# Kernel optimization log

Hardware: AMD Instinct MI355X
Metric: run time of the kernel (lower is better)

The kernel has to match this reference:

```python
import jax, jax.numpy as jnp
from jax import lax
import numpy as np
import math

EMBED_DIM = 1024
NUM_HEADS = 16
REDUCTION = 2


def setup_inputs() -> dict:
    key = jax.random.key(0)
    ks = jax.random.split(key, 11)
    B, N, C = 2, 4096, EMBED_DIM
    s = 1.0 / math.sqrt(C)
    return {
        "x": jax.random.normal(ks[0], (B, N, C), jnp.float32),
        "q_w": jax.random.normal(ks[1], (C, C), jnp.float32) * s,
        "q_b": jax.random.normal(ks[2], (C,), jnp.float32) * s,
        "k_w": jax.random.normal(ks[3], (C, C), jnp.float32) * s,
        "k_b": jax.random.normal(ks[4], (C,), jnp.float32) * s,
        "v_w": jax.random.normal(ks[5], (C, C), jnp.float32) * s,
        "v_b": jax.random.normal(ks[6], (C,), jnp.float32) * s,
        "conv_w": jax.random.normal(ks[7], (C, 1, 3), jnp.float32) * 0.5,
        "conv_b": jax.random.normal(ks[8], (C,), jnp.float32) * 0.1,
        "out_w": jax.random.normal(ks[9], (C, C), jnp.float32) * s,
        "out_b": jax.random.normal(ks[10], (C,), jnp.float32) * s,
    }


def reference(x, q_w, q_b, k_w, k_b, v_w, v_b, conv_w, conv_b, out_w, out_b):
    B, N, C = x.shape
    H = NUM_HEADS
    D = C // H
    scale = 1.0 / math.sqrt(D)

    q = x @ q_w.T + q_b  # [B,N,C]

    # depthwise conv1d KV downsample: kernel=3, stride=REDUCTION, pad=1, groups=C
    xd = jnp.transpose(x, (0, 2, 1))  # [B,C,N]
    xd = lax.conv_general_dilated(
        xd, conv_w, window_strides=(REDUCTION,), padding=[(1, 1)],
        feature_group_count=C, dimension_numbers=("NCH", "OIH", "NCH"))
    xd = xd + conv_b[None, :, None]
    xd = jnp.transpose(xd, (0, 2, 1))  # [B,Nk,C]

    k = xd @ k_w.T + k_b
    v = xd @ v_w.T + v_b

    Nk = k.shape[1]
    q = q.reshape(B, N, H, D).transpose(0, 2, 1, 3)   # [B,H,N,D]
    k = k.reshape(B, Nk, H, D).transpose(0, 2, 1, 3)  # [B,H,Nk,D]
    v = v.reshape(B, Nk, H, D).transpose(0, 2, 1, 3)

    att = jnp.einsum("bhnd,bhmd->bhnm", q, k) * scale  # [B,H,N,Nk]
    att = jax.nn.softmax(att, axis=-1)
    out = jnp.einsum("bhnm,bhmd->bhnd", att, v)        # [B,H,N,D]
    out = out.transpose(0, 2, 1, 3).reshape(B, N, C)
    return out @ out_w.T + out_b
```

## Files before the change

### kernel.cpp

```cpp
#include <hip/hip_runtime.h>
#include <stdint.h>
#include <stddef.h>


using bf16x8 = __attribute__((ext_vector_type(8))) short;
using f32x4  = __attribute__((ext_vector_type(4))) float;
using f32x16 = __attribute__((ext_vector_type(16))) float;
using u16x4  = __attribute__((ext_vector_type(4))) unsigned short;
using u32x4  = __attribute__((ext_vector_type(4))) uint32_t;

#if defined(__has_builtin)
#if __has_builtin(__builtin_amdgcn_exp2f)
#define FAST_EXP2(x) __builtin_amdgcn_exp2f(x)
#endif
#endif
#ifndef FAST_EXP2
extern "C" __device__ float __ocml_native_exp2_f32(float);
#define FAST_EXP2(x) __ocml_native_exp2_f32(x)
#endif

__device__ __forceinline__ unsigned short f2bf(float f) {
  union { float f; uint32_t u; } v; v.f = f;
  uint32_t r = v.u + 0x7fffu + ((v.u >> 16) & 1u);
  return (unsigned short)(r >> 16);
}

__device__ __forceinline__ uint32_t cvt_pk_bf16(float lo, float hi) {
  uint32_t r;
  asm("v_cvt_pk_bf16_f32 %0, %1, %2" : "=v"(r) : "v"(lo), "v"(hi));
  return r;
}

__device__ __forceinline__ void plane32_swap(uint32_t& a, uint32_t& b) {
  asm("v_permlane32_swap_b32 %0, %1" : "+v"(a), "+v"(b));
}

__global__ __launch_bounds__(256)
void cast_bf16_kernel(const float* __restrict__ in, unsigned short* __restrict__ out, int n) {
  int i = (blockIdx.x * 256 + threadIdx.x) * 8;
  if (i >= n) return;
  float4 a = *(const float4*)(in + i);
  float4 b = *(const float4*)(in + i + 4);
  u16x4 r0 = {f2bf(a.x), f2bf(a.y), f2bf(a.z), f2bf(a.w)};
  u16x4 r1 = {f2bf(b.x), f2bf(b.y), f2bf(b.z), f2bf(b.w)};
  *(u16x4*)(out + i) = r0;
  *(u16x4*)(out + i + 4) = r1;
}

struct WPtrs { const float* p0; const float* p1; const float* p2; const float* p3; };
__global__ __launch_bounds__(256)
void cast4_bf16_kernel(WPtrs in, unsigned short* __restrict__ out) {
  int which = blockIdx.x >> 9;
  int i = ((blockIdx.x & 511) * 256 + threadIdx.x) * 8;
  const float* src = (which == 0) ? in.p0 : (which == 1) ? in.p1
                   : (which == 2) ? in.p2 : in.p3;
  unsigned short* dst = out + (size_t)which * 1048576;
  float4 a = *(const float4*)(src + i);
  float4 b = *(const float4*)(src + i + 4);
  u16x4 r0 = {f2bf(a.x), f2bf(a.y), f2bf(a.z), f2bf(a.w)};
  u16x4 r1 = {f2bf(b.x), f2bf(b.y), f2bf(b.z), f2bf(b.w)};
  *(u16x4*)(dst + i) = r0;
  *(u16x4*)(dst + i + 4) = r1;
}

__global__ __launch_bounds__(256)
void conv_ds_kernel(const float* __restrict__ x, const float* __restrict__ cw,
                    const float* __restrict__ cb, unsigned short* __restrict__ xd) {
  int row = blockIdx.x;
  int b = row >> 11, m = row & 2047;
  int c = threadIdx.x * 4;
  const float* xb = x + (size_t)b * 4096 * 1024;
  int n0 = 2 * m - 1;
  float4 x0 = {0.f, 0.f, 0.f, 0.f};
  if (n0 >= 0) x0 = *(const float4*)(xb + (size_t)n0 * 1024 + c);
  float4 x1 = *(const float4*)(xb + (size_t)(2 * m) * 1024 + c);
  float4 x2 = *(const float4*)(xb + (size_t)(2 * m + 1) * 1024 + c);
  float4 w0 = *(const float4*)(cw + c * 3);
  float4 w1 = *(const float4*)(cw + c * 3 + 4);
  float4 w2 = *(const float4*)(cw + c * 3 + 8);
  float4 bb = *(const float4*)(cb + c);
  float r0 = x0.x * w0.x + x1.x * w0.y + x2.x * w0.z + bb.x;
  float r1 = x0.y * w0.w + x1.y * w1.x + x2.y * w1.y + bb.y;
  float r2 = x0.z * w1.z + x1.z * w1.w + x2.z * w2.x + bb.z;
  float r3 = x0.w * w2.y + x1.w * w2.z + x2.w * w2.w + bb.w;
  u16x4 r = {f2bf(r0), f2bf(r1), f2bf(r2), f2bf(r3)};
  *(u16x4*)(xd + (size_t)row * 1024 + c) = r;
}

template<int OUT_MODE>
__global__ __launch_bounds__(256)
void gemm_bt(const unsigned short* __restrict__ A, const unsigned short* __restrict__ W,
             const float* __restrict__ bias, const float* __restrict__ bias2,
             void* __restrict__ out, void* __restrict__ out2,
             int M, int N, int K) {
  __shared__ unsigned short As[128 * 32];
  __shared__ unsigned short Bs[128 * 32];
  const int tid = threadIdx.x;
  const int w = tid >> 6, lane = tid & 63;
  const int nbn = N >> 7;
  const int bm = blockIdx.x / nbn, bn = blockIdx.x % nbn;
  const int wr = w >> 1, wc = w & 1;
  const int l15 = lane & 15, l4 = lane >> 4;

  f32x4 acc[4][4];
#pragma unroll
  for (int m = 0; m < 4; ++m)
#pragma unroll
    for (int n = 0; n < 4; ++n) acc[m][n] = (f32x4)0.0f;

  const int arow = bm * 128 + w * 16 + (lane >> 2);
  const int brow = bn * 128 + w * 16 + (lane >> 2);
  const int kcol = (lane & 3) * 8;

  for (int kt = 0; kt < K; kt += 32) {
#pragma unroll
    for (int p = 0; p < 2; ++p) {
      __builtin_amdgcn_global_load_lds(
          (const __attribute__((address_space(1))) void*)(A + (size_t)(arow + p * 64) * K + kt + kcol),
          (__attribute__((address_space(3))) void*)(As + p * 2048 + w * 512), 16, 0, 0);
      __builtin_amdgcn_global_load_lds(
          (const __attribute__((address_space(1))) void*)(W + (size_t)(brow + p * 64) * K + kt + kcol),
          (__attribute__((address_space(3))) void*)(Bs + p * 2048 + w * 512), 16, 0, 0);
    }
    __syncthreads();
    bf16x8 af[4], bf[4];
#pragma unroll
    for (int m = 0; m < 4; ++m) af[m] = *(const bf16x8*)(As + (wr * 64 + m * 16 + l15) * 32 + l4 * 8);
#pragma unroll
    for (int n = 0; n < 4; ++n) bf[n] = *(const bf16x8*)(Bs + (wc * 64 + n * 16 + l15) * 32 + l4 * 8);
#pragma unroll
    for (int m = 0; m < 4; ++m)
#pragma unroll
      for (int n = 0; n < 4; ++n)
        acc[m][n] = __builtin_amdgcn_mfma_f32_16x16x32_bf16(af[m], bf[n], acc[m][n], 0, 0, 0);
    __syncthreads();
  }

  const bool vregion = (OUT_MODE == 3) && (bn >= 8);
#pragma unroll
  for (int n = 0; n < 4; ++n) {
    int col = bn * 128 + wc * 64 + n * 16 + l15;
    float bv = vregion ? bias2[col - 1024] : bias[col];
#pragma unroll
    for (int m = 0; m < 4; ++m) {
      int row0 = bm * 128 + wr * 64 + m * 16 + l4 * 4;
      if (vregion) {
        int b = row0 >> 11, kv = row0 & 2047;
        u16x4 r = {f2bf(acc[m][n][0] + bv), f2bf(acc[m][n][1] + bv),
                   f2bf(acc[m][n][2] + bv), f2bf(acc[m][n][3] + bv)};
        *(u16x4*)((unsigned short*)out2 + ((size_t)(b * 1024 + (col - 1024))) * 2048 + kv) = r;
      } else if (OUT_MODE == 1 || OUT_MODE == 3) {
        const int ldn = (OUT_MODE == 3) ? 1024 : N;
#pragma unroll
        for (int i = 0; i < 4; ++i)
          ((unsigned short*)out)[(size_t)(row0 + i) * ldn + col] = f2bf(acc[m][n][i] + bv);
      } else {
#pragma unroll
        for (int i = 0; i < 4; ++i)
          ((float*)out)[(size_t)(row0 + i) * N + col] = acc[m][n][i] + bv;
      }
    }
  }
}

#define ATT_SCL_L2E 0.18033688011112043f

__global__ __launch_bounds__(256)
void flash_attn_kernel(const unsigned short* __restrict__ q,
                       const unsigned short* __restrict__ k,
                       const unsigned short* __restrict__ vt,
                       unsigned short* __restrict__ o) {
  const int bid = blockIdx.x;
  const int lin = (bid & 7) * 128 + (bid >> 3);
  const int qb = lin & 31;
  const int hb = lin >> 5;
  const int h = hb & 15, b = hb >> 4;

  const int tid = threadIdx.x;
  const int w = tid >> 6, lane = tid & 63;
  const int l31 = lane & 31, hi = lane >> 5;

  __shared__ unsigned short Ks[2][64 * 64];
  __shared__ unsigned short Vs[2][64 * 64];

  const size_t C = 1024;
  const int qrow = b * 4096 + qb * 128 + w * 32 + l31;

  bf16x8 qf[4];
#pragma unroll
  for (int ks = 0; ks < 4; ++ks)
    qf[ks] = *(const bf16x8*)(q + (size_t)qrow * C + h * 64 + ks * 16 + hi * 8);

  f32x16 o0 = (f32x16)0.0f, o1 = (f32x16)0.0f;
  float lrun = 0.f;

  const int srow = (tid & 7) | ((tid >> 5) << 3);
  const int sc2  = (tid >> 3) & 3;
  const int sxor = (srow & 7);
  const unsigned short* kbase = k  + ((size_t)(b * 2048 + srow)) * C + h * 64;
  const unsigned short* vbase = vt + ((size_t)(b * 1024 + h * 64 + srow)) * 2048;

  const int r0 = l31, r1 = 32 + l31;
  const int x0c = (r0 & 7) * 8, x1c = (r1 & 7) * 8;

  auto exppack = [&](f32x16& s0, f32x16& s1, u32x4 (&pw)[4]) {
    float rs0 = 0.f, rs1 = 0.f;
#pragma unroll
    for (int i = 0; i < 16; ++i) {
      float p0 = FAST_EXP2(s0[i] * ATT_SCL_L2E);
      float p1 = FAST_EXP2(s1[i] * ATT_SCL_L2E);
      s0[i] = p0; s1[i] = p1;
      rs0 += p0; rs1 += p1;
    }
    lrun += rs0 + rs1;
#pragma unroll
    for (int hh = 0; hh < 2; ++hh) {
#pragma unroll
      for (int cp = 0; cp < 2; ++cp) {
#pragma unroll
        for (int e = 0; e < 2; ++e) {
          float xa0 = (hh == 0) ? s0[8 * cp + 2 * e]     : s1[8 * cp + 2 * e];
          float xa1 = (hh == 0) ? s0[8 * cp + 2 * e + 1] : s1[8 * cp + 2 * e + 1];
          float xb0 = (hh == 0) ? s0[8 * cp + 4 + 2 * e]     : s1[8 * cp + 4 + 2 * e];
          float xb1 = (hh == 0) ? s0[8 * cp + 4 + 2 * e + 1] : s1[8 * cp + 4 + 2 * e + 1];
          uint32_t wa = cvt_pk_bf16(xa0, xa1);
          uint32_t wb = cvt_pk_bf16(xb0, xb1);
          plane32_swap(wa, wb);
          pw[2 * hh + cp][e]     = wa;
          pw[2 * hh + cp][e + 2] = wb;
        }
      }
    }
  };

  bf16x8 krg[2], vrg[2], tmp[2];
#pragma unroll
  for (int j = 0; j < 2; ++j) tmp[j] = *(const bf16x8*)(kbase + (sc2 + 4 * j) * 8);
#pragma unroll
  for (int j = 0; j < 2; ++j)
    *(bf16x8*)(&Ks[0][srow * 64 + (((sc2 + 4 * j) ^ sxor) * 8)]) = tmp[j];
#pragma unroll
  for (int j = 0; j < 2; ++j) tmp[j] = *(const bf16x8*)(kbase + (size_t)64 * C + (sc2 + 4 * j) * 8);
#pragma unroll
  for (int j = 0; j < 2; ++j)
    *(bf16x8*)(&Ks[1][srow * 64 + (((sc2 + 4 * j) ^ sxor) * 8)]) = tmp[j];
#pragma unroll
  for (int j = 0; j < 2; ++j) tmp[j] = *(const bf16x8*)(vbase + (sc2 + 4 * j) * 8);
#pragma unroll
  for (int j = 0; j < 2; ++j)
    *(bf16x8*)(&Vs[0][srow * 64 + (((sc2 + 4 * j) ^ sxor) * 8)]) = tmp[j];
#pragma unroll
  for (int j = 0; j < 2; ++j) {
    krg[j] = *(const bf16x8*)(kbase + (size_t)128 * C + (sc2 + 4 * j) * 8);
    vrg[j] = *(const bf16x8*)(vbase + 64 + (sc2 + 4 * j) * 8);
  }
  __syncthreads();

  u32x4 pwA[4], pwB[4];
  {
    f32x16 s0 = (f32x16)0.0f, s1 = (f32x16)0.0f;
    __builtin_amdgcn_s_setprio(1);
#pragma unroll
    for (int ks = 0; ks < 4; ++ks) {
      int coff = ks * 16 + hi * 8;
      bf16x8 kf0 = *(const bf16x8*)(&Ks[0][r0 * 64 + (coff ^ x0c)]);
      bf16x8 kf1 = *(const bf16x8*)(&Ks[0][r1 * 64 + (coff ^ x1c)]);
      s0 = __builtin_amdgcn_mfma_f32_32x32x16_bf16(kf0, qf[ks], s0, 0, 0, 0);
      s1 = __builtin_amdgcn_mfma_f32_32x32x16_bf16(kf1, qf[ks], s1, 0, 0, 0);
    }
    __builtin_amdgcn_s_setprio(0);
    exppack(s0, s1, pwA);
  }
  __syncthreads();

  auto body = [&](int t, u32x4 (&pwC)[4], u32x4 (&pwN)[4]) {
    const unsigned short* Vc = Vs[t & 1];
    f32x16 s0 = (f32x16)0.0f, s1 = (f32x16)0.0f;

    __builtin_amdgcn_s_setprio(1);
    if (t < 31) {
      const unsigned short* Kn = Ks[(t + 1) & 1];
#pragma unroll
      for (int ks = 0; ks < 4; ++ks) {
        int coff = ks * 16 + hi * 8;
        bf16x8 kf0 = *(const bf16x8*)(Kn + r0 * 64 + (coff ^ x0c));
        bf16x8 kf1 = *(const bf16x8*)(Kn + r1 * 64 + (coff ^ x1c));
        s0 = __builtin_amdgcn_mfma_f32_32x32x16_bf16(kf0, qf[ks], s0, 0, 0, 0);
        s1 = __builtin_amdgcn_mfma_f32_32x32x16_bf16(kf1, qf[ks], s1, 0, 0, 0);
      }
    }
#pragma unroll
    for (int ksv = 0; ksv < 4; ++ksv) {
      bf16x8 pv = __builtin_bit_cast(bf16x8, pwC[ksv]);
      int coff = ksv * 16 + hi * 8;
      bf16x8 vf0 = *(const bf16x8*)(Vc + r0 * 64 + (coff ^ x0c));
      bf16x8 vf1 = *(const bf16x8*)(Vc + r1 * 64 + (coff ^ x1c));
      o0 = __builtin_amdgcn_mfma_f32_32x32x16_bf16(vf0, pv, o0, 0, 0, 0);
      o1 = __builtin_amdgcn_mfma_f32_32x32x16_bf16(vf1, pv, o1, 0, 0, 0);
    }
    __builtin_amdgcn_s_setprio(0);

    if (t < 30) {
#pragma unroll
      for (int j = 0; j < 2; ++j)
        *(bf16x8*)(&((unsigned short*)Ks[t & 1])[srow * 64 + (((sc2 + 4 * j) ^ sxor) * 8)]) = krg[j];
    }
    if (t < 31) {
#pragma unroll
      for (int j = 0; j < 2; ++j)
        *(bf16x8*)(&((unsigned short*)Vs[(t + 1) & 1])[srow * 64 + (((sc2 + 4 * j) ^ sxor) * 8)]) = vrg[j];
    }
    if (t < 29) {
#pragma unroll
      for (int j = 0; j < 2; ++j)
        krg[j] = *(const bf16x8*)(kbase + (size_t)(t + 3) * 64 * C + (sc2 + 4 * j) * 8);
    }
    if (t < 30) {
#pragma unroll
      for (int j = 0; j < 2; ++j)
        vrg[j] = *(const bf16x8*)(vbase + (t + 2) * 64 + (sc2 + 4 * j) * 8);
    }

    if (t < 31) exppack(s0, s1, pwN);

    if (t < 31) __syncthreads();
  };

  for (int tt = 0; tt < 16; ++tt) {
    body(2 * tt,     pwA, pwB);
    body(2 * tt + 1, pwB, pwA);
  }

  float lsum = lrun + __shfl_xor(lrun, 32);
  const float inv = 1.0f / lsum;
  u32x4 ow[4];
#pragma unroll
  for (int c = 0; c < 4; ++c) {
#pragma unroll
    for (int e = 0; e < 2; ++e) {
      uint32_t wa = cvt_pk_bf16(o0[4 * c + 2 * e] * inv, o0[4 * c + 2 * e + 1] * inv);
      uint32_t wb = cvt_pk_bf16(o1[4 * c + 2 * e] * inv, o1[4 * c + 2 * e + 1] * inv);
      plane32_swap(wa, wb);
      ow[c][e]     = wa;
      ow[c][e + 2] = wb;
    }
  }
  unsigned short* op = o + (size_t)qrow * C + h * 64 + hi * 32;
#pragma unroll
  for (int ch = 0; ch < 4; ++ch)
    *(u32x4*)(op + ch * 8) = ow[ch];
}

extern "C" void kernel_launch(void* const* d_in, const int* in_sizes, int n_in,
                              void* d_out, int out_size, void* d_ws, size_t ws_size,
                              hipStream_t stream) {
  const float* x   = (const float*)d_in[0];
  const float* q_w = (const float*)d_in[1];
  const float* q_b = (const float*)d_in[2];
  const float* k_w = (const float*)d_in[3];
  const float* k_b = (const float*)d_in[4];
  const float* v_w = (const float*)d_in[5];
  const float* v_b = (const float*)d_in[6];
  const float* cw  = (const float*)d_in[7];
  const float* cb  = (const float*)d_in[8];
  const float* o_w = (const float*)d_in[9];
  const float* o_b = (const float*)d_in[10];
  float* out = (float*)d_out;

  unsigned short* ws    = (unsigned short*)d_ws;
  unsigned short* x_bf  = ws;
  unsigned short* qw_bf = x_bf + 8388608;
  unsigned short* kw_bf = qw_bf + 1048576;
  unsigned short* vw_bf = kw_bf + 1048576;
  unsigned short* ow_bf = vw_bf + 1048576;
  unsigned short* q_bf  = ow_bf + 1048576;
  unsigned short* xd_bf = q_bf + 8388608;
  unsigned short* k_bf  = xd_bf + 4194304;
  unsigned short* vt_bf = k_bf + 4194304;
  unsigned short* ao_bf = x_bf;

  cast_bf16_kernel<<<4096, 256, 0, stream>>>(x, x_bf, 8388608);
  WPtrs wp = {q_w, k_w, v_w, o_w};
  cast4_bf16_kernel<<<2048, 256, 0, stream>>>(wp, qw_bf);
  conv_ds_kernel<<<4096, 256, 0, stream>>>(x, cw, cb, xd_bf);

  gemm_bt<1><<<512, 256, 0, stream>>>(x_bf, qw_bf, q_b, nullptr, q_bf, nullptr,
                                      8192, 1024, 1024);
  gemm_bt<3><<<512, 256, 0, stream>>>(xd_bf, kw_bf, k_b, v_b, k_bf, vt_bf,
                                      4096, 2048, 1024);

  flash_attn_kernel<<<1024, 256, 0, stream>>>(q_bf, k_bf, vt_bf, ao_bf);

  gemm_bt<0><<<512, 256, 0, stream>>>(ao_bf, ow_bf, o_b, nullptr, out, nullptr,
                                      8192, 1024, 1024);
}
```

Before: 208.3 us.

## Double query rows per wave in flash attention and fold softmax scale into Q GEMM

Each wave now processes 64 query rows (two 32-row groups) instead of 32, so every K/V tile loaded into shared memory is reused across twice as many queries. The attention grid halves from 1024 to 512 blocks. The softmax scale times log2(e) is applied in the Q projection epilogue, which removes a multiply per score in the exp loop. In exchange, register pressure rises roughly twofold (more accumulators and packed P), occupancy may drop, and 512 blocks may underfill the GPU's compute units.

Measured after the change: 211.8 us. Within noise of the previous version (+1.7%).

```diff
diff --git a/kernel.cpp b/kernel.cpp
--- a/kernel.cpp
+++ b/kernel.cpp
@@ -8,6 +8,8 @@
 using f32x16 = __attribute__((ext_vector_type(16))) float;
 using u16x4  = __attribute__((ext_vector_type(4))) unsigned short;
 using u32x4  = __attribute__((ext_vector_type(4))) uint32_t;
+
+#define ATT_SCL_L2E 0.18033688011112043f
 
 #if defined(__has_builtin)
 #if __has_builtin(__builtin_amdgcn_exp2f)
@@ -149,11 +151,15 @@
         u16x4 r = {f2bf(acc[m][n][0] + bv), f2bf(acc[m][n][1] + bv),
                    f2bf(acc[m][n][2] + bv), f2bf(acc[m][n][3] + bv)};
         *(u16x4*)((unsigned short*)out2 + ((size_t)(b * 1024 + (col - 1024))) * 2048 + kv) = r;
-      } else if (OUT_MODE == 1 || OUT_MODE == 3) {
-        const int ldn = (OUT_MODE == 3) ? 1024 : N;
+      } else if (OUT_MODE == 1) {
 #pragma unroll
         for (int i = 0; i < 4; ++i)
-          ((unsigned short*)out)[(size_t)(row0 + i) * ldn + col] = f2bf(acc[m][n][i] + bv);
+          ((unsigned short*)out)[(size_t)(row0 + i) * N + col] =
+              f2bf((acc[m][n][i] + bv) * ATT_SCL_L2E);
+      } else if (OUT_MODE == 3) {
+#pragma unroll
+        for (int i = 0; i < 4; ++i)
+          ((unsigned short*)out)[(size_t)(row0 + i) * 1024 + col] = f2bf(acc[m][n][i] + bv);
       } else {
 #pragma unroll
         for (int i = 0; i < 4; ++i)
@@ -162,8 +168,6 @@
     }
   }
 }
-
-#define ATT_SCL_L2E 0.18033688011112043f
 
 __global__ __launch_bounds__(256)
 void flash_attn_kernel(const unsigned short* __restrict__ q,
@@ -171,9 +175,9 @@
                        const unsigned short* __restrict__ vt,
                        unsigned short* __restrict__ o) {
   const int bid = blockIdx.x;
-  const int lin = (bid & 7) * 128 + (bid >> 3);
-  const int qb = lin & 31;
-  const int hb = lin >> 5;
+  const int lin = (bid & 7) * 64 + (bid >> 3);
+  const int qb = lin & 15;
+  const int hb = lin >> 4;
   const int h = hb & 15, b = hb >> 4;
 
   const int tid = threadIdx.x;
@@ -184,15 +188,19 @@
   __shared__ unsigned short Vs[2][64 * 64];
 
   const size_t C = 1024;
-  const int qrow = b * 4096 + qb * 128 + w * 32 + l31;
-
-  bf16x8 qf[4];
-#pragma unroll
-  for (int ks = 0; ks < 4; ++ks)
-    qf[ks] = *(const bf16x8*)(q + (size_t)qrow * C + h * 64 + ks * 16 + hi * 8);
-
-  f32x16 o0 = (f32x16)0.0f, o1 = (f32x16)0.0f;
-  float lrun = 0.f;
+  const int qrow0 = b * 4096 + qb * 256 + w * 64;
+  const int rqA = qrow0 + l31, rqB = qrow0 + 32 + l31;
+
+  bf16x8 qfA[4], qfB[4];
+#pragma unroll
+  for (int ks = 0; ks < 4; ++ks) {
+    qfA[ks] = *(const bf16x8*)(q + (size_t)rqA * C + h * 64 + ks * 16 + hi * 8);
+    qfB[ks] = *(const bf16x8*)(q + (size_t)rqB * C + h * 64 + ks * 16 + hi * 8);
+  }
+
+  f32x16 o0A = (f32x16)0.0f, o1A = (f32x16)0.0f;
+  f32x16 o0B = (f32x16)0.0f, o1B = (f32x16)0.0f;
+  float lrunA = 0.f, lrunB = 0.f;
 
   const int srow = (tid & 7) | ((tid >> 5) << 3);
   const int sc2  = (tid >> 3) & 3;
@@ -203,31 +211,38 @@
   const int r0 = l31, r1 = 32 + l31;
   const int x0c = (r0 & 7) * 8, x1c = (r1 & 7) * 8;
 
-  auto exppack = [&](f32x16& s0, f32x16& s1, u32x4 (&pw)[4]) {
-    float rs0 = 0.f, rs1 = 0.f;
+  auto exppack = [&](f32x16& a0, f32x16& a1, f32x16& b0, f32x16& b1, u32x4 (&pw)[8]) {
+    float rsA = 0.f, rsB = 0.f;
 #pragma unroll
     for (int i = 0; i < 16; ++i) {
-      float p0 = FAST_EXP2(s0[i] * ATT_SCL_L2E);
-      float p1 = FAST_EXP2(s1[i] * ATT_SCL_L2E);
-      s0[i] = p0; s1[i] = p1;
-      rs0 += p0; rs1 += p1;
-    }
-    lrun += rs0 + rs1;
-#pragma unroll
-    for (int hh = 0; hh < 2; ++hh) {
-#pragma unroll
-      for (int cp = 0; cp < 2; ++cp) {
-#pragma unroll
-        for (int e = 0; e < 2; ++e) {
-          float xa0 = (hh == 0) ? s0[8 * cp + 2 * e]     : s1[8 * cp + 2 * e];
-          float xa1 = (hh == 0) ? s0[8 * cp + 2 * e + 1] : s1[8 * cp + 2 * e + 1];
-          float xb0 = (hh == 0) ? s0[8 * cp + 4 + 2 * e]     : s1[8 * cp + 4 + 2 * e];
-          float xb1 = (hh == 0) ? s0[8 * cp + 4 + 2 * e + 1] : s1[8 * cp + 4 + 2 * e + 1];
-          uint32_t wa = cvt_pk_bf16(xa0, xa1);
-          uint32_t wb = cvt_pk_bf16(xb0, xb1);
-          plane32_swap(wa, wb);
-          pw[2 * hh + cp][e]     = wa;
-          pw[2 * hh + cp][e + 2] = wb;
+      float pa0 = FAST_EXP2(a0[i]);
+      float pa1 = FAST_EXP2(a1[i]);
+      float pb0 = FAST_EXP2(b0[i]);
+      float pb1 = FAST_EXP2(b1[i]);
+      a0[i] = pa0; a1[i] = pa1; b0[i] = pb0; b1[i] = pb1;
+      rsA += pa0 + pa1; rsB += pb0 + pb1;
+    }
+    lrunA += rsA; lrunB += rsB;
+#pragma unroll
+    for (int g = 0; g < 2; ++g) {
+      f32x16& s0 = g ? b0 : a0;
+      f32x16& s1 = g ? b1 : a1;
+#pragma unroll
+      for (int hh = 0; hh < 2; ++hh) {
+#pragma unroll
+        for (int cp = 0; cp < 2; ++cp) {
+#pragma unroll
+          for (int e = 0; e < 2; ++e) {
+            float xa0 = (hh == 0) ? s0[8 * cp + 2 * e]     : s1[8 * cp + 2 * e];
+            float xa1 = (hh == 0) ? s0[8 * cp + 2 * e + 1] : s1[8 * cp + 2 * e + 1];
+            float xb0 = (hh == 0) ? s0[8 * cp + 4 + 2 * e]     : s1[8 * cp + 4 + 2 * e];
+            float xb1 = (hh == 0) ? s0[8 * cp + 4 + 2 * e + 1] : s1[8 * cp + 4 + 2 * e + 1];
+            uint32_t wa = cvt_pk_bf16(xa0, xa1);
+            uint32_t wb = cvt_pk_bf16(xb0, xb1);
+            plane32_swap(wa, wb);
+            pw[g * 4 + 2 * hh + cp][e]     = wa;
+            pw[g * 4 + 2 * hh + cp][e + 2] = wb;
+          }
         }
       }
     }
@@ -256,26 +271,30 @@
   }
   __syncthreads();
 
-  u32x4 pwA[4], pwB[4];
+  u32x4 pwA[8], pwB[8];
   {
-    f32x16 s0 = (f32x16)0.0f, s1 = (f32x16)0.0f;
+    f32x16 sA0 = (f32x16)0.0f, sA1 = (f32x16)0.0f;
+    f32x16 sB0 = (f32x16)0.0f, sB1 = (f32x16)0.0f;
     __builtin_amdgcn_s_setprio(1);
 #pragma unroll
     for (int ks = 0; ks < 4; ++ks) {
       int coff = ks * 16 + hi * 8;
       bf16x8 kf0 = *(const bf16x8*)(&Ks[0][r0 * 64 + (coff ^ x0c)]);
       bf16x8 kf1 = *(const bf16x8*)(&Ks[0][r1 * 64 + (coff ^ x1c)]);
-      s0 = __builtin_amdgcn_mfma_f32_32x32x16_bf16(kf0, qf[ks], s0, 0, 0, 0);
-      s1 = __builtin_amdgcn_mfma_f32_32x32x16_bf16(kf1, qf[ks], s1, 0, 0, 0);
+      sA0 = __builtin_amdgcn_mfma_f32_32x32x16_bf16(kf0, qfA[ks], sA0, 0, 0, 0);
+      sA1 = __builtin_amdgcn_mfma_f32_32x32x16_bf16(kf1, qfA[ks], sA1, 0, 0, 0);
+      sB0 = __builtin_amdgcn_mfma_f32_32x32x16_bf16(kf0, qfB[ks], sB0, 0, 0, 0);
+      sB1 = __builtin_amdgcn_mfma_f32_32x32x16_bf16(kf1, qfB[ks], sB1, 0, 0, 0);
     }
     __builtin_amdgcn_s_setprio(0);
-    exppack(s0, s1, pwA);
+    exppack(sA0, sA1, sB0, sB1, pwA);
   }
   __syncthreads();
 
-  auto body = [&](int t, u32x4 (&pwC)[4], u32x4 (&pwN)[4]) {
+  auto body = [&](int t, u32x4 (&pwC)[8], u32x4 (&pwN)[8]) {
     const unsigned short* Vc = Vs[t & 1];
-    f32x16 s0 = (f32x16)0.0f, s1 = (f32x16)0.0f;
+    f32x16 sA0 = (f32x16)0.0f, sA1 = (f32x16)0.0f;
+    f32x16 sB0 = (f32x16)0.0f, sB1 = (f32x16)0.0f;
 
     __builtin_amdgcn_s_setprio(1);
     if (t < 31) {
@@ -285,18 +304,23 @@
         int coff = ks * 16 + hi * 8;
         bf16x8 kf0 = *(const bf16x8*)(Kn + r0 * 64 + (coff ^ x0c));
         bf16x8 kf1 = *(const bf16x8*)(Kn + r1 * 64 + (coff ^ x1c));
-        s0 = __builtin_amdgcn_mfma_f32_32x32x16_bf16(kf0, qf[ks], s0, 0, 0, 0);
-        s1 = __builtin_amdgcn_mfma_f32_32x32x16_bf16(kf1, qf[ks], s1, 0, 0, 0);
+        sA0 = __builtin_amdgcn_mfma_f32_32x32x16_bf16(kf0, qfA[ks], sA0, 0, 0, 0);
+        sA1 = __builtin_amdgcn_mfma_f32_32x32x16_bf16(kf1, qfA[ks], sA1, 0, 0, 0);
+        sB0 = __builtin_amdgcn_mfma_f32_32x32x16_bf16(kf0, qfB[ks], sB0, 0, 0, 0);
+        sB1 = __builtin_amdgcn_mfma_f32_32x32x16_bf16(kf1, qfB[ks], sB1, 0, 0, 0);
       }
     }
 #pragma unroll
     for (int ksv = 0; ksv < 4; ++ksv) {
-      bf16x8 pv = __builtin_bit_cast(bf16x8, pwC[ksv]);
+      bf16x8 pvA = __builtin_bit_cast(bf16x8, pwC[ksv]);
+      bf16x8 pvB = __builtin_bit_cast(bf16x8, pwC[4 + ksv]);
       int coff = ksv * 16 + hi * 8;
       bf16x8 vf0 = *(const bf16x8*)(Vc + r0 * 64 + (coff ^ x0c));
       bf16x8 vf1 = *(const bf16x8*)(Vc + r1 * 64 + (coff ^ x1c));
-      o0 = __builtin_amdgcn_mfma_f32_32x32x16_bf16(vf0, pv, o0, 0, 0, 0);
-      o1 = __builtin_amdgcn_mfma_f32_32x32x16_bf16(vf1, pv, o1, 0, 0, 0);
+      o0A = __builtin_amdgcn_mfma_f32_32x32x16_bf16(vf0, pvA, o0A, 0, 0, 0);
+      o1A = __builtin_amdgcn_mfma_f32_32x32x16_bf16(vf1, pvA, o1A, 0, 0, 0);
+      o0B = __builtin_amdgcn_mfma_f32_32x32x16_bf16(vf0, pvB, o0B, 0, 0, 0);
+      o1B = __builtin_amdgcn_mfma_f32_32x32x16_bf16(vf1, pvB, o1B, 0, 0, 0);
     }
     __builtin_amdgcn_s_setprio(0);
 
@@ -321,7 +345,7 @@
         vrg[j] = *(const bf16x8*)(vbase + (t + 2) * 64 + (sc2 + 4 * j) * 8);
     }
 
-    if (t < 31) exppack(s0, s1, pwN);
+    if (t < 31) exppack(sA0, sA1, sB0, sB1, pwN);
 
     if (t < 31) __syncthreads();
   };
@@ -331,24 +355,28 @@
     body(2 * tt + 1, pwB, pwA);
   }
 
-  float lsum = lrun + __shfl_xor(lrun, 32);
-  const float inv = 1.0f / lsum;
-  u32x4 ow[4];
-#pragma unroll
-  for (int c = 0; c < 4; ++c) {
-#pragma unroll
-    for (int e = 0; e < 2; ++e) {
-      uint32_t wa = cvt_pk_bf16(o0[4 * c + 2 * e] * inv, o0[4 * c + 2 * e + 1] * inv);
-      uint32_t wb = cvt_pk_bf16(o1[4 * c + 2 * e] * inv, o1[4 * c + 2 * e + 1] * inv);
-      plane32_swap(wa, wb);
-      ow[c][e]     = wa;
-      ow[c][e + 2] = wb;
-    }
-  }
-  unsigned short* op = o + (size_t)qrow * C + h * 64 + hi * 32;
-#pragma unroll
-  for (int ch = 0; ch < 4; ++ch)
-    *(u32x4*)(op + ch * 8) = ow[ch];
+  auto store_group = [&](f32x16& g0, f32x16& g1, float lrun, int row) {
+    float lsum = lrun + __shfl_xor(lrun, 32);
+    const float inv = 1.0f / lsum;
+    u32x4 ow[4];
+#pragma unroll
+    for (int c = 0; c < 4; ++c) {
+#pragma unroll
+      for (int e = 0; e < 2; ++e) {
+        uint32_t wa = cvt_pk_bf16(g0[4 * c + 2 * e] * inv, g0[4 * c + 2 * e + 1] * inv);
+        uint32_t wb = cvt_pk_bf16(g1[4 * c + 2 * e] * inv, g1[4 * c + 2 * e + 1] * inv);
+        plane32_swap(wa, wb);
+        ow[c][e]     = wa;
+        ow[c][e + 2] = wb;
+      }
+    }
+    unsigned short* op = o + (size_t)row * C + h * 64 + hi * 32;
+#pragma unroll
+    for (int ch = 0; ch < 4; ++ch)
+      *(u32x4*)(op + ch * 8) = ow[ch];
+  };
+  store_group(o0A, o1A, lrunA, rqA);
+  store_group(o0B, o1B, lrunB, rqB);
 }
 
 extern "C" void kernel_launch(void* const* d_in, const int* in_sizes, int n_in,
@@ -389,7 +417,7 @@
   gemm_bt<3><<<512, 256, 0, stream>>>(xd_bf, kw_bf, k_b, v_b, k_bf, vt_bf,
                                       4096, 2048, 1024);
 
-  flash_attn_kernel<<<1024, 256, 0, stream>>>(q_bf, k_bf, vt_bf, ao_bf);
+  flash_attn_kernel<<<512, 256, 0, stream>>>(q_bf, k_bf, vt_bf, ao_bf);
 
   gemm_bt<0><<<512, 256, 0, stream>>>(ao_bf, ow_bf, o_b, nullptr, out, nullptr,
                                       8192, 1024, 1024);
```
